# Performance work log

Hardware: AMD Instinct MI355X
Metric: run time of the kernel (lower is better)

Reference implementation:

```python
import jax, jax.numpy as jnp
import numpy as np

B, N, DIM = 4, 2048, 1024
HEADS, DIM_HEAD = 16, 64
INNER = HEADS * DIM_HEAD
SCALE = DIM_HEAD ** -0.5


def setup_inputs() -> dict:
    key = jax.random.key(0)
    k1, k2, k3 = jax.random.split(key, 3)
    x = jax.random.normal(k1, (B, N, DIM), dtype=jnp.float32)
    w_qkv = jax.random.normal(k2, (DIM, 3 * INNER), dtype=jnp.float32) * (DIM ** -0.5)
    w_out = jax.random.normal(k3, (INNER, DIM), dtype=jnp.float32) * (INNER ** -0.5)
    b_out = jnp.zeros((DIM,), dtype=jnp.float32)
    return {"x": x, "w_qkv": w_qkv, "w_out": w_out, "b_out": b_out}


def reference(x, w_qkv, w_out, b_out):
    # qkv projection: [B, N, 3*inner]
    qkv = jnp.einsum('bnd,de->bne', x, w_qkv)
    q, k, v = jnp.split(qkv, 3, axis=-1)
    # 'b n (h d) -> b h n d'
    split_heads = lambda t: t.reshape(B, N, HEADS, DIM_HEAD).transpose(0, 2, 1, 3)
    q, k, v = split_heads(q), split_heads(k), split_heads(v)
    dots = jnp.einsum('bhid,bhjd->bhij', q, k) * SCALE  # [B, H, N, N]
    attn = jax.nn.softmax(dots, axis=-1)
    out = jnp.einsum('bhij,bhjd->bhid', attn, v)
    # 'b h n d -> b n (h d)'
    out = out.transpose(0, 2, 1, 3).reshape(B, N, INNER)
    out = jnp.einsum('bne,ed->bnd', out, w_out) + b_out
    return out
```

## Files before the change

### kernel.cpp

```cpp
#include <hip/hip_runtime.h>
#include <hip/hip_bf16.h>
#include <stdint.h>

typedef float f32x4 __attribute__((ext_vector_type(4)));
typedef float f32x16 __attribute__((ext_vector_type(16)));
typedef short s16x8 __attribute__((ext_vector_type(8)));
typedef unsigned u32x4 __attribute__((ext_vector_type(4)));
typedef unsigned short us16;

#define LOG2E 1.44269504088896340736f

__device__ __forceinline__ us16 f2b(float f) {
  union { float f; unsigned u; } v; v.f = f;
  return (us16)((v.u + 0x7fffu + ((v.u >> 16) & 1u)) >> 16);
}

__device__ __forceinline__ unsigned cvtpk(float lo, float hi) {
  unsigned r;
  asm("v_cvt_pk_bf16_f32 %0, %1, %2" : "=v"(r) : "v"(lo), "v"(hi));
  return r;
}

__device__ __forceinline__ void plswap(unsigned& a, unsigned& b) {
  asm volatile("v_permlane32_swap_b32 %0, %1" : "+v"(a), "+v"(b));
}

__device__ __forceinline__ void gload16(const void* g, void* l) {
  __builtin_amdgcn_global_load_lds((__attribute__((address_space(1))) void*)g,
                                   (__attribute__((address_space(3))) void*)l,
                                   16, 0, 0);
}

#define MFMA16(acc, a, b) \
  (acc) = __builtin_amdgcn_mfma_f32_16x16x32_bf16((a), (b), (acc), 0, 0, 0)
#define MFMA32(acc, a, b) \
  (acc) = __builtin_amdgcn_mfma_f32_32x32x16_bf16((a), (b), (acc), 0, 0, 0)

__global__ void convx_kernel(const float* __restrict__ x, us16* __restrict__ xb) {
  const int idx = blockIdx.x * 256 + threadIdx.x;
  const float4 v = ((const float4*)x)[idx];
  ushort4 o;
  o.x = f2b(v.x); o.y = f2b(v.y); o.z = f2b(v.z); o.w = f2b(v.w);
  ((ushort4*)xb)[idx] = o;
}

__global__ void convw_kernel(const float* __restrict__ wqkv, const float* __restrict__ wout,
                             us16* __restrict__ wqkvT, us16* __restrict__ woutT) {
  __shared__ float tile[64][65];
  const int bid = blockIdx.x;
  const bool isq = bid < 768;
  const int j = isq ? bid : bid - 768;
  const int ntiles = isq ? 48 : 16;
  const int nt = j % ntiles, kt = j / ntiles;
  const int NN = isq ? 3072 : 1024;
  const float* W = isq ? wqkv : wout;
  us16* WT = isq ? wqkvT : woutT;
  const int n0 = nt * 64, k0 = kt * 64;
  const int t = threadIdx.x;
  const int tc = t & 63, tr = t >> 6;
#pragma unroll
  for (int p = 0; p < 16; ++p)
    tile[p * 4 + tr][tc] = W[(size_t)(k0 + p * 4 + tr) * NN + n0 + tc];
  __syncthreads();
#pragma unroll
  for (int p = 0; p < 16; ++p) {
    const int nl = p * 4 + tr;
    float v = tile[tc][nl];
    if (isq && (n0 + nl) < 1024) v *= 0.125f * LOG2E;
    WT[(size_t)(n0 + nl) * 1024 + k0 + tc] = f2b(v);
  }
}

__global__ __launch_bounds__(512, 2)
void gemm8p(const us16* __restrict__ A, const us16* __restrict__ Bm,
            us16* __restrict__ C) {
  __shared__ us16 As[2][2][128 * 64];
  __shared__ us16 Bs[2][128 * 64];
  const int t = threadIdx.x;
  const int l = t & 63;
  const int lr = l & 15, lh = l >> 4;
  const int w = t >> 6;
  const int wm = w >> 1, wn = w & 1;

  const int bid = blockIdx.x;
  const int swz = (bid & 7) * 96 + (bid >> 3);
  const size_t m0 = (size_t)(swz & 31) * 256;
  const size_t n0 = (size_t)(swz >> 5) * 128;

  f32x4 acc[4][4] = {};

  auto stage = [&](us16* dst, const us16* src, size_t rb, int kt2) {
    if (kt2 < 16) {
#pragma unroll
      for (int i2 = 0; i2 < 2; ++i2) {
        const int e = i2 * 512 + t;
        const int row = e >> 3, slot = e & 7;
        gload16(src + (rb + row) * 1024 + kt2 * 64 + ((slot ^ (row & 7)) << 3),
                dst + e * 8);
      }
    }
  };

  stage(&As[0][0][0], A, m0, 0);
  stage(&As[0][1][0], A, m0 + 128, 0);
  stage(&Bs[0][0], Bm, n0, 0);
  stage(&Bs[1][0], Bm, n0, 1);
  asm volatile("s_waitcnt vmcnt(0)" ::: "memory");
  asm volatile("s_barrier" ::: "memory");

  const int ahalf = wm >> 1;
  const int arow0 = (wm & 1) * 64;
  const int brow0 = wn * 64;

  for (int it = 0; it < 8; ++it) {
    const int T = 2 * it;
    s16x8 bv[4][2];
#pragma unroll
    for (int p = 0; p < 4; ++p) {
      const int tb = p >> 1;
      const int q = p & 1;
      const us16* aP = &As[tb][ahalf][0];
      const us16* bP = &Bs[tb][0];
      s16x8 av[2][2];
#pragma unroll
      for (int j = 0; j < 2; ++j)
#pragma unroll
        for (int ks = 0; ks < 2; ++ks) {
          const int row = arow0 + (2 * q + j) * 16 + lr;
          const int slot = (ks * 4 + lh) ^ (lr & 7);
          av[j][ks] = *(const s16x8*)&aP[row * 64 + slot * 8];
        }
      if (q == 0) {
#pragma unroll
        for (int fc = 0; fc < 4; ++fc)
#pragma unroll
          for (int ks = 0; ks < 2; ++ks) {
            const int row = brow0 + fc * 16 + lr;
            const int slot = (ks * 4 + lh) ^ (lr & 7);
            bv[fc][ks] = *(const s16x8*)&bP[row * 64 + slot * 8];
          }
      }
      switch (p) {
        case 0: stage(&As[1][0][0], A, m0, T + 1);
                stage(&As[1][1][0], A, m0 + 128, T + 1); break;
        case 1: stage(&Bs[0][0], Bm, n0, T + 2); break;
        case 2: stage(&As[0][0][0], A, m0, T + 2);
                stage(&As[0][1][0], A, m0 + 128, T + 2); break;
        case 3: stage(&Bs[1][0], Bm, n0, T + 3); break;
      }
      asm volatile("s_barrier" ::: "memory");
      __builtin_amdgcn_s_setprio(1);
#pragma unroll
      for (int fc = 0; fc < 4; ++fc)
#pragma unroll
        for (int j = 0; j < 2; ++j)
#pragma unroll
          for (int ks = 0; ks < 2; ++ks)
            MFMA16(acc[2 * q + j][fc], av[j][ks], bv[fc][ks]);
      __builtin_amdgcn_s_setprio(0);
      if (p == 1 || p == 3) {
        if (it == 7) { asm volatile("s_waitcnt vmcnt(0)" ::: "memory"); }
        else         { asm volatile("s_waitcnt vmcnt(2)" ::: "memory"); }
      }
      asm volatile("s_barrier" ::: "memory");
    }
  }
#pragma unroll
  for (int fr = 0; fr < 4; ++fr) {
    const size_t r0 = m0 + wm * 64 + fr * 16 + lh * 4;
#pragma unroll
    for (int fc = 0; fc < 4; ++fc) {
      const size_t col = n0 + wn * 64 + fc * 16 + lr;
#pragma unroll
      for (int rg = 0; rg < 4; ++rg)
        C[(r0 + rg) * 3072 + col] = f2b(acc[fr][fc][rg]);
    }
  }
}

template <int OUT_BF16>
__global__ __launch_bounds__(256, 2)
void gemm_bt(const us16* __restrict__ A, const us16* __restrict__ B,
             void* __restrict__ C, const float* __restrict__ bias, int N) {
  __shared__ us16 sm[2][2][128 * 64];
  const int t = threadIdx.x;
  const int l = t & 63;
  const int lr = l & 15, lh = l >> 4;
  const int w = t >> 6;
  const int wm = w >> 1, wn = w & 1;
  const int bm = blockIdx.x & 63;
  const int bn = blockIdx.x >> 6;
  const size_t m0 = (size_t)bm * 128, n0 = (size_t)bn * 128;

  f32x4 acc[4][4] = {};

  auto stage = [&](int buf, int kt) {
    const int k0 = kt << 6;
#pragma unroll
    for (int i = 0; i < 4; ++i) {
      const int e = i * 256 + t;
      const int r = e >> 3, c = (e & 7) << 3;
      gload16(A + (m0 + r) * 1024 + k0 + c, &sm[buf][0][e * 8]);
      gload16(B + (n0 + r) * 1024 + k0 + c, &sm[buf][1][e * 8]);
    }
  };

  stage(0, 0);
  __syncthreads();
  int cur = 0;
  for (int kt = 0; kt < 16; ++kt) {
    if (kt < 15) stage(cur ^ 1, kt + 1);
    const us16* sA = &sm[cur][0][0];
    const us16* sB = &sm[cur][1][0];
#pragma unroll
    for (int kk = 0; kk < 64; kk += 32) {
      s16x8 av[4], bv[4];
#pragma unroll
      for (int i = 0; i < 4; ++i)
        av[i] = *(const s16x8*)&sA[(wm * 64 + i * 16 + lr) * 64 + kk + lh * 8];
#pragma unroll
      for (int jj = 0; jj < 4; ++jj)
        bv[jj] = *(const s16x8*)&sB[(wn * 64 + jj * 16 + lr) * 64 + kk + lh * 8];
#pragma unroll
      for (int i = 0; i < 4; ++i)
#pragma unroll
        for (int jj = 0; jj < 4; ++jj)
          MFMA16(acc[i][jj], av[i], bv[jj]);
    }
    __syncthreads();
    cur ^= 1;
  }
#pragma unroll
  for (int i = 0; i < 4; ++i) {
    const size_t row0 = m0 + wm * 64 + i * 16 + lh * 4;
#pragma unroll
    for (int jj = 0; jj < 4; ++jj) {
      const size_t col = n0 + wn * 64 + jj * 16 + lr;
#pragma unroll
      for (int r = 0; r < 4; ++r) {
        const float v = acc[i][jj][r];
        if constexpr (OUT_BF16) {
          ((us16*)C)[(row0 + r) * N + col] = f2b(v);
        } else {
          ((float*)C)[(row0 + r) * N + col] = v + bias[col];
        }
      }
    }
  }
}

__global__ __launch_bounds__(512)
void attn_kernel(const us16* __restrict__ qkv, us16* __restrict__ attno) {
  __shared__ us16 Klds[2][64 * 64];
  __shared__ us16 Vt[2][64 * 64];
  const int tid = threadIdx.x;
  const int l31 = tid & 31;
  const int hi = (tid >> 5) & 1;
  const int w = tid >> 6;

  const int bid = blockIdx.x;
  const int bh = (bid & 7) * 8 + (bid >> 5);
  const int qt = (bid >> 3) & 3;
  const int b = bh >> 4, h = bh & 15;

  const size_t rowbase = (size_t)b * 2048;
  const int kcol = 1024 + h * 64, vcol = 2048 + h * 64;
  const size_t qrow0 = rowbase + qt * 512 + w * 64;

  s16x8 qa[4], qb[4];
  {
    const us16* qpa = qkv + (qrow0 + l31) * 3072 + h * 64 + hi * 8;
    const us16* qpb = qkv + (qrow0 + 32 + l31) * 3072 + h * 64 + hi * 8;
#pragma unroll
    for (int s = 0; s < 4; ++s) {
      qa[s] = *(const s16x8*)(qpa + s * 16);
      qb[s] = *(const s16x8*)(qpb + s * 16);
    }
  }

  const int tid4 = tid - 256;
  const int kvv = (tid & 31) * 2;
  const int vd0 = ((tid >> 5) & 7) * 8;
  auto stageK = [&](int buf, int kt2) {
#pragma unroll
    for (int i = 0; i < 2; ++i) {
      const int e = i * 256 + tid4;
      const int kv = e >> 3, sl = e & 7;
      gload16(qkv + (rowbase + (size_t)kt2 * 64 + kv) * 3072 + kcol + ((sl ^ (kv & 7)) << 3),
              &Klds[buf][e * 8]);
    }
  };
  auto vload = [&](int kt2, s16x8& a, s16x8& c) {
    const us16* vp = qkv + (rowbase + (size_t)kt2 * 64 + kvv) * 3072 + vcol + vd0;
    a = *(const s16x8*)vp;
    c = *(const s16x8*)(vp + 3072);
  };
  auto vwrite = [&](int buf, const s16x8 a, const s16x8 c) {
#pragma unroll
    for (int i = 0; i < 8; ++i) {
      const int row = vd0 + i;
      const unsigned pk = (unsigned)(us16)a[i] | ((unsigned)(us16)c[i] << 16);
      *(unsigned*)&Vt[buf][row * 64 + (kvv ^ ((row & 7) << 3))] = pk;
    }
  };

  f32x16 oA0 = {}, oA1 = {}, oB0 = {}, oB1 = {};
  float lsA = 0.0f, lsB = 0.0f;

  s16x8 vna, vnc;
  if (w < 4) { vload(0, vna, vnc); vwrite(0, vna, vnc); }
  else stageK(0, 0);
  __syncthreads();

  for (int kt = 0; kt < 32; ++kt) {
    const int cur = kt & 1;
    if (kt < 31) {
      if (w < 4) vload(kt + 1, vna, vnc);
      else stageK(cur ^ 1, kt + 1);
    }

    const us16* Kb = &Klds[cur][0];
    s16x8 kf0, kf1, kf2, kf3, kf4, kf5, kf6, kf7;
    {
      const int x7 = l31 & 7;
      kf0 = *(const s16x8*)&Kb[l31 * 64 + (((0 + hi) ^ x7) << 3)];
      kf1 = *(const s16x8*)&Kb[(32 + l31) * 64 + (((0 + hi) ^ x7) << 3)];
      kf2 = *(const s16x8*)&Kb[l31 * 64 + (((2 + hi) ^ x7) << 3)];
      kf3 = *(const s16x8*)&Kb[(32 + l31) * 64 + (((2 + hi) ^ x7) << 3)];
      kf4 = *(const s16x8*)&Kb[l31 * 64 + (((4 + hi) ^ x7) << 3)];
      kf5 = *(const s16x8*)&Kb[(32 + l31) * 64 + (((4 + hi) ^ x7) << 3)];
      kf6 = *(const s16x8*)&Kb[l31 * 64 + (((6 + hi) ^ x7) << 3)];
      kf7 = *(const s16x8*)&Kb[(32 + l31) * 64 + (((6 + hi) ^ x7) << 3)];
    }

    s16x8 paA[4], paB[4];
    {
      f32x16 st0 = {}, st1 = {};
      __builtin_amdgcn_s_setprio(1);
      MFMA32(st0, kf0, qa[0]); MFMA32(st1, kf1, qa[0]);
      MFMA32(st0, kf2, qa[1]); MFMA32(st1, kf3, qa[1]);
      MFMA32(st0, kf4, qa[2]); MFMA32(st1, kf5, qa[2]);
      MFMA32(st0, kf6, qa[3]); MFMA32(st1, kf7, qa[3]);
      __builtin_amdgcn_s_setprio(0);
      float ps = 0.0f;
#pragma unroll
      for (int r = 0; r < 16; ++r) {
        st0[r] = __builtin_amdgcn_exp2f(st0[r]);
        st1[r] = __builtin_amdgcn_exp2f(st1[r]);
        ps += st0[r] + st1[r];
      }
      lsA += ps;
#pragma unroll
      for (int half = 0; half < 2; ++half) {
        const f32x16& sp = half ? st1 : st0;
#pragma unroll
        for (int g = 0; g < 2; ++g) {
          unsigned a0 = cvtpk(sp[8 * g + 0], sp[8 * g + 1]);
          unsigned a1 = cvtpk(sp[8 * g + 2], sp[8 * g + 3]);
          unsigned b0 = cvtpk(sp[8 * g + 4], sp[8 * g + 5]);
          unsigned b1 = cvtpk(sp[8 * g + 6], sp[8 * g + 7]);
          plswap(a0, b0);
          plswap(a1, b1);
          union { u32x4 u; s16x8 s; } cv;
          cv.u = (u32x4){a0, a1, b0, b1};
          paA[2 * half + g] = cv.s;
        }
      }
    }
    {
      f32x16 st0 = {}, st1 = {};
      __builtin_amdgcn_s_setprio(1);
      MFMA32(st0, kf0, qb[0]); MFMA32(st1, kf1, qb[0]);
      MFMA32(st0, kf2, qb[1]); MFMA32(st1, kf3, qb[1]);
      MFMA32(st0, kf4, qb[2]); MFMA32(st1, kf5, qb[2]);
      MFMA32(st0, kf6, qb[3]); MFMA32(st1, kf7, qb[3]);
      __builtin_amdgcn_s_setprio(0);
      float ps = 0.0f;
#pragma unroll
      for (int r = 0; r < 16; ++r) {
        st0[r] = __builtin_amdgcn_exp2f(st0[r]);
        st1[r] = __builtin_amdgcn_exp2f(st1[r]);
        ps += st0[r] + st1[r];
      }
      lsB += ps;
#pragma unroll
      for (int half = 0; half < 2; ++half) {
        const f32x16& sp = half ? st1 : st0;
#pragma unroll
        for (int g = 0; g < 2; ++g) {
          unsigned a0 = cvtpk(sp[8 * g + 0], sp[8 * g + 1]);
          unsigned a1 = cvtpk(sp[8 * g + 2], sp[8 * g + 3]);
          unsigned b0 = cvtpk(sp[8 * g + 4], sp[8 * g + 5]);
          unsigned b1 = cvtpk(sp[8 * g + 6], sp[8 * g + 7]);
          plswap(a0, b0);
          plswap(a1, b1);
          union { u32x4 u; s16x8 s; } cv;
          cv.u = (u32x4){a0, a1, b0, b1};
          paB[2 * half + g] = cv.s;
        }
      }
    }

    const us16* Vb = &Vt[cur][0];
    __builtin_amdgcn_s_setprio(1);
#pragma unroll
    for (int ks = 0; ks < 4; ++ks) {
      const int sl = ((2 * ks + hi) ^ (l31 & 7)) << 3;
      const s16x8 vb0 = *(const s16x8*)&Vb[l31 * 64 + sl];
      const s16x8 vb1 = *(const s16x8*)&Vb[(32 + l31) * 64 + sl];
      MFMA32(oA0, paA[ks], vb0); MFMA32(oA1, paA[ks], vb1);
      MFMA32(oB0, paB[ks], vb0); MFMA32(oB1, paB[ks], vb1);
    }
    __builtin_amdgcn_s_setprio(0);

    if (kt < 31 && w < 4) vwrite(cur ^ 1, vna, vnc);
    __syncthreads();
  }

  const float lA = lsA + __shfl_xor(lsA, 32);
  const float lB = lsB + __shfl_xor(lsB, 32);
  const float liA = 1.0f / lA, liB = 1.0f / lB;
#pragma unroll
  for (int r = 0; r < 16; ++r) {
    const int q = (r & 3) + 8 * (r >> 2) + 4 * hi;
    const float fA = __shfl(liA, q);
    const float fB = __shfl(liB, q);
    const size_t rowA = qrow0 + q;
    const size_t rowB = qrow0 + 32 + q;
    attno[rowA * 1024 + h * 64 + l31] = f2b(oA0[r] * fA);
    attno[rowA * 1024 + h * 64 + 32 + l31] = f2b(oA1[r] * fA);
    attno[rowB * 1024 + h * 64 + l31] = f2b(oB0[r] * fB);
    attno[rowB * 1024 + h * 64 + 32 + l31] = f2b(oB1[r] * fB);
  }
}

extern "C" void kernel_launch(void* const* d_in, const int* in_sizes, int n_in,
                              void* d_out, int out_size, void* d_ws, size_t ws_size,
                              hipStream_t stream) {
  (void)in_sizes; (void)n_in; (void)out_size;
  const float* x     = (const float*)d_in[0];
  const float* w_qkv = (const float*)d_in[1];
  const float* w_out = (const float*)d_in[2];
  const float* b_out = (const float*)d_in[3];

  if (ws_size < 92274688u) return;
  char* ws = (char*)d_ws;
  us16* xb    = (us16*)(ws);
  us16* wqkvT = (us16*)(ws + 16777216);
  us16* woutT = (us16*)(ws + 23068672);
  us16* qkv   = (us16*)(ws + 25165824);
  us16* attno = (us16*)(ws + 75497472);

  convx_kernel<<<8192, 256, 0, stream>>>(x, xb);
  convw_kernel<<<1024, 256, 0, stream>>>(w_qkv, w_out, wqkvT, woutT);
  gemm8p<<<768, 512, 0, stream>>>(xb, wqkvT, qkv);
  attn_kernel<<<256, 512, 0, stream>>>(qkv, attno);
  gemm_bt<0><<<512, 256, 0, stream>>>(attno, woutT, d_out, b_out, 1024);
}
```

Baseline: 199.1 us.

## Triple-buffer QKV GEMM LDS tiles to prefetch two K-steps ahead

```diff
diff --git a/kernel.cpp b/kernel.cpp
--- a/kernel.cpp
+++ b/kernel.cpp
@@ -74,8 +74,8 @@
 __global__ __launch_bounds__(512, 2)
 void gemm8p(const us16* __restrict__ A, const us16* __restrict__ Bm,
             us16* __restrict__ C) {
-  __shared__ us16 As[2][2][128 * 64];
-  __shared__ us16 Bs[2][128 * 64];
+  __shared__ us16 As[3][2][128 * 64];
+  __shared__ us16 Bs[3][128 * 64];
   const int t = threadIdx.x;
   const int l = t & 63;
   const int lr = l & 15, lh = l >> 4;
@@ -100,37 +100,38 @@
       }
     }
   };
-
-  stage(&As[0][0][0], A, m0, 0);
-  stage(&As[0][1][0], A, m0 + 128, 0);
-  stage(&Bs[0][0], Bm, n0, 0);
-  stage(&Bs[1][0], Bm, n0, 1);
-  asm volatile("s_waitcnt vmcnt(0)" ::: "memory");
+  auto stageA = [&](int buf, int kt2) {
+    stage(&As[buf][0][0], A, m0, kt2);
+    stage(&As[buf][1][0], A, m0 + 128, kt2);
+  };
+  auto stageB = [&](int buf, int kt2) { stage(&Bs[buf][0], Bm, n0, kt2); };
+
+  stageA(0, 0); stageB(0, 0);
+  stageA(1, 1); stageB(1, 1);
+  asm volatile("s_waitcnt vmcnt(6)" ::: "memory");
   asm volatile("s_barrier" ::: "memory");
 
   const int ahalf = wm >> 1;
   const int arow0 = (wm & 1) * 64;
   const int brow0 = wn * 64;
 
-  for (int it = 0; it < 8; ++it) {
-    const int T = 2 * it;
+  for (int kt = 0; kt < 16; ++kt) {
+    const int tb = kt % 3, sb = (kt + 2) % 3;
+    const us16* aP = &As[tb][ahalf][0];
+    const us16* bP = &Bs[tb][0];
     s16x8 bv[4][2];
 #pragma unroll
-    for (int p = 0; p < 4; ++p) {
-      const int tb = p >> 1;
-      const int q = p & 1;
-      const us16* aP = &As[tb][ahalf][0];
-      const us16* bP = &Bs[tb][0];
+    for (int p = 0; p < 2; ++p) {
       s16x8 av[2][2];
 #pragma unroll
       for (int j = 0; j < 2; ++j)
 #pragma unroll
         for (int ks = 0; ks < 2; ++ks) {
-          const int row = arow0 + (2 * q + j) * 16 + lr;
+          const int row = arow0 + (2 * p + j) * 16 + lr;
           const int slot = (ks * 4 + lh) ^ (lr & 7);
           av[j][ks] = *(const s16x8*)&aP[row * 64 + slot * 8];
         }
-      if (q == 0) {
+      if (p == 0) {
 #pragma unroll
         for (int fc = 0; fc < 4; ++fc)
 #pragma unroll
@@ -140,14 +141,8 @@
             bv[fc][ks] = *(const s16x8*)&bP[row * 64 + slot * 8];
           }
       }
-      switch (p) {
-        case 0: stage(&As[1][0][0], A, m0, T + 1);
-                stage(&As[1][1][0], A, m0 + 128, T + 1); break;
-        case 1: stage(&Bs[0][0], Bm, n0, T + 2); break;
-        case 2: stage(&As[0][0][0], A, m0, T + 2);
-                stage(&As[0][1][0], A, m0 + 128, T + 2); break;
-        case 3: stage(&Bs[1][0], Bm, n0, T + 3); break;
-      }
+      if (p == 0) stageA(sb, kt + 2);
+      else        stageB(sb, kt + 2);
       asm volatile("s_barrier" ::: "memory");
       __builtin_amdgcn_s_setprio(1);
 #pragma unroll
@@ -156,11 +151,11 @@
         for (int j = 0; j < 2; ++j)
 #pragma unroll
           for (int ks = 0; ks < 2; ++ks)
-            MFMA16(acc[2 * q + j][fc], av[j][ks], bv[fc][ks]);
+            MFMA16(acc[2 * p + j][fc], av[j][ks], bv[fc][ks]);
       __builtin_amdgcn_s_setprio(0);
-      if (p == 1 || p == 3) {
-        if (it == 7) { asm volatile("s_waitcnt vmcnt(0)" ::: "memory"); }
-        else         { asm volatile("s_waitcnt vmcnt(2)" ::: "memory"); }
+      if (p == 1) {
+        if (kt >= 14) { asm volatile("s_waitcnt vmcnt(0)" ::: "memory"); }
+        else          { asm volatile("s_waitcnt vmcnt(6)" ::: "memory"); }
       }
       asm volatile("s_barrier" ::: "memory");
     }
```

Result: faster. 191.2 us (-4.0%).
